# Kernel optimization log

Measured on AMD Instinct MI355X. Metric: run time of the kernel, lower is better.

Reference implementation:

```python
import jax, jax.numpy as jnp
import numpy as np

DIM = 768
HEADS = 12
HD = DIM // HEADS
SCALE = float(np.sqrt(HD))  # sqrt(dim // num_heads)


def layernorm(x, g, b, eps=1e-5):
    m = jnp.mean(x, axis=-1, keepdims=True)
    v = jnp.var(x, axis=-1, keepdims=True)
    return (x - m) * jax.lax.rsqrt(v + eps) * g + b


def dwconv(x, w, b, pad):
    # x: [B,C,H,W], w: [C,1,kh,kw] depthwise
    y = jax.lax.conv_general_dilated(
        x, w, window_strides=(1, 1), padding=[(pad, pad), (pad, pad)],
        feature_group_count=x.shape[1], dimension_numbers=('NCHW', 'OIHW', 'NCHW'))
    return y + b[None, :, None, None]


def mha(xq, xkv, wq, bq, wk, bk, wv, bv, wo, bo):
    # per-head Linears batched over heads; wq/wk/wv: [H, C, hd], biases [H, hd]
    B, N, C = xq.shape
    q = jnp.einsum('bnc,hcd->bhnd', xq, wq) + bq[None, :, None, :]
    k = jnp.einsum('bnc,hcd->bhnd', xkv, wk) + bk[None, :, None, :]
    v = jnp.einsum('bnc,hcd->bhnd', xkv, wv) + bv[None, :, None, :]
    z = jax.nn.sigmoid(jnp.einsum('bhnd,bhmd->bhnm', q, k) / SCALE)  # sigmoid, not softmax
    o = jnp.einsum('bhnm,bhmd->bhnd', z, v)
    o = o.transpose(0, 2, 1, 3).reshape(B, N, C)  # concat heads along feature dim
    return o @ wo + bo


def reference(decoder, wq1, bq1, wk1, bk1, wv1, bv1, wo1, bo1,
              wq2, bq2, wk2, bk2, wv2, bv2, wo2, bo2,
              alphas1, alphas2, peg_w, peg_b,
              ln1_g, ln1_b, ln2_g, ln2_b,
              cn_dw_w, cn_dw_b, cn_ln_g, cn_ln_b,
              cn_w1, cn_b1, cn_w2, cn_b2, cn_scale, cn_alphas):
    B, C, H, W = decoder.shape
    x = decoder.transpose(0, 2, 3, 1).reshape(B, H * W, C)  # [B,N,C]
    # block 1: alpha * x + MHA(x,x,x)
    x = alphas1 * x + mha(x, x, wq1, bq1, wk1, bk1, wv1, bv1, wo1, bo1)
    # PEG: depthwise 3x3 conv (replaces x, no residual in source)
    x4 = x.reshape(B, H, W, C).transpose(0, 3, 1, 2)
    x4 = dwconv(x4, peg_w, peg_b, pad=1)
    x = x4.transpose(0, 2, 3, 1).reshape(B, H * W, C)
    x = layernorm(x, ln1_g, ln1_b)
    # block 2 (encoder is None -> self-attention)
    x = alphas2 * x + mha(x, x, wq2, bq2, wk2, bk2, wv2, bv2, wo2, bo2)
    x = layernorm(x, ln2_g, ln2_b)
    x4 = x.reshape(B, H, W, C).transpose(0, 3, 1, 2)  # [B,C,H,W]
    # CNBlock head: dwconv7x7 -> LN -> Linear(4d) -> GELU -> Linear(d), layer_scale + alpha residual
    y = dwconv(x4, cn_dw_w, cn_dw_b, pad=3)
    y = y.transpose(0, 2, 3, 1)  # [B,H,W,C]
    y = layernorm(y, cn_ln_g, cn_ln_b)
    y = jax.nn.gelu(y @ cn_w1 + cn_b1, approximate=False)
    y = y @ cn_w2 + cn_b2
    y = y.transpose(0, 3, 1, 2)  # [B,C,H,W]
    out = cn_scale[None, :, None, None] * y + x4 * cn_alphas[None, :, None, None]
    return out


def setup_inputs() -> dict:
    key = jax.random.key(0)
    ks = iter(jax.random.split(key, 40))
    def n(shape, s=0.02):
        return jax.random.normal(next(ks), shape, dtype=jnp.float32) * s
    d = {}
    d['decoder'] = jax.random.normal(next(ks), (8, DIM, 32, 32), dtype=jnp.float32)
    for i in (1, 2):
        d[f'wq{i}'] = n((HEADS, DIM, HD)); d[f'bq{i}'] = n((HEADS, HD), 1e-6)
        d[f'wk{i}'] = n((HEADS, DIM, HD)); d[f'bk{i}'] = n((HEADS, HD), 1e-6)
        d[f'wv{i}'] = n((HEADS, DIM, HD)); d[f'bv{i}'] = n((HEADS, HD), 1e-6)
        d[f'wo{i}'] = n((DIM, DIM)); d[f'bo{i}'] = n((DIM,), 1e-6)
    d['alphas1'] = jnp.ones((DIM,), jnp.float32)
    d['alphas2'] = jnp.ones((DIM,), jnp.float32)
    d['peg_w'] = n((DIM, 1, 3, 3), 0.1); d['peg_b'] = n((DIM,), 1e-6)
    d['ln1_g'] = jnp.ones((DIM,), jnp.float32); d['ln1_b'] = jnp.zeros((DIM,), jnp.float32)
    d['ln2_g'] = jnp.ones((DIM,), jnp.float32); d['ln2_b'] = jnp.zeros((DIM,), jnp.float32)
    d['cn_dw_w'] = n((DIM, 1, 7, 7), 0.1); d['cn_dw_b'] = n((DIM,), 0.02)
    d['cn_ln_g'] = jnp.ones((DIM,), jnp.float32); d['cn_ln_b'] = jnp.zeros((DIM,), jnp.float32)
    d['cn_w1'] = n((DIM, 4 * DIM)); d['cn_b1'] = n((4 * DIM,), 0.02)
    d['cn_w2'] = n((4 * DIM, DIM)); d['cn_b2'] = n((DIM,), 0.02)
    d['cn_scale'] = jnp.full((DIM,), 1e-6, jnp.float32)
    d['cn_alphas'] = jnp.ones((DIM,), jnp.float32)
    return d
```

## Files before the change

kernel.cpp:

```cpp
#include <hip/hip_runtime.h>
#include <math.h>

#define BATCH 8
#define CDIM 768
#define NTOK 1024
#define NH 12
#define HDIM 64
#define QKVN 2304

typedef __attribute__((ext_vector_type(8))) short bf16x8;
typedef __attribute__((ext_vector_type(4))) float f32x4;

__device__ inline short f2bf(float f) {
    union { float f; unsigned u; } v; v.f = f;
    unsigned r = (v.u + 0x7FFF + ((v.u >> 16) & 1)) >> 16;
    return (short)r;
}

__device__ inline unsigned pack2bf(float lo, float hi) {
    return (unsigned)(unsigned short)f2bf(lo) | ((unsigned)(unsigned short)f2bf(hi) << 16);
}

__device__ inline void async_copy16(const short* g, short* l) {
    __builtin_amdgcn_global_load_lds(
        (const __attribute__((address_space(1))) void*)g,
        (__attribute__((address_space(3))) void*)l, 16, 0, 0);
}

__global__ __launch_bounds__(256) void k_prep(
    const float* __restrict__ wq1, const float* __restrict__ wk1, const float* __restrict__ wv1,
    const float* __restrict__ wq2, const float* __restrict__ wk2, const float* __restrict__ wv2,
    const float* __restrict__ wo1, const float* __restrict__ wo2,
    const float* __restrict__ cnw1, const float* __restrict__ cnw2,
    const float* __restrict__ bq1, const float* __restrict__ bk1, const float* __restrict__ bv1,
    const float* __restrict__ bq2, const float* __restrict__ bk2, const float* __restrict__ bv2,
    const float* __restrict__ dec,
    short* __restrict__ Wqkv1, short* __restrict__ Wqkv2,
    short* __restrict__ WoT1, short* __restrict__ WoT2,
    short* __restrict__ W1T, short* __restrict__ W2T,
    float* __restrict__ bqkv1, float* __restrict__ bqkv2,
    float* __restrict__ A0, short* __restrict__ Xb) {
    __shared__ float sh[64 * 65];
    int bid = blockIdx.x;
    int t = threadIdx.x;
    if (bid < 864) {
        int bx = bid % 12, z = bid / 12;
        int set = z / 36, rem = z % 36, sect = rem / 12, hh = rem % 12;
        const float* srcs[6] = {wq1, wk1, wv1, wq2, wk2, wv2};
        const float* src = srcs[set * 3 + sect] + (size_t)hh * 768 * 64;
        short* dst = (set ? Wqkv2 : Wqkv1) + ((size_t)sect * 768 + hh * 64) * 768;
        int k0 = bx * 64;
#pragma unroll
        for (int p = 0; p < 16; ++p) {
            int gid = t + p * 256;
            int r = gid >> 6, c = gid & 63;
            sh[r * 65 + c] = src[(size_t)(k0 + r) * 64 + c];
        }
        __syncthreads();
#pragma unroll
        for (int p = 0; p < 16; ++p) {
            int gid = t + p * 256;
            int d = gid >> 6, kk = gid & 63;
            dst[(size_t)d * 768 + k0 + kk] = f2bf(sh[kk * 65 + d]);
        }
    } else if (bid < 6624) {
        int r = bid - 864;
        const float* src; short* dst; int R, C, bx, by;
        if (r < 576)       { src = wo1;  dst = WoT1; R = 768;  C = 768;  bx = r % 24; by = r / 24; }
        else if (r < 1152) { int s = r - 576;  src = wo2;  dst = WoT2; R = 768;  C = 768;  bx = s % 24; by = s / 24; }
        else if (r < 3456) { int s = r - 1152; src = cnw1; dst = W1T;  R = 768;  C = 3072; bx = s % 96; by = s / 96; }
        else               { int s = r - 3456; src = cnw2; dst = W2T;  R = 3072; C = 768;  bx = s % 24; by = s / 24; }
        int c0 = bx * 32, r0 = by * 32, tx = t & 31, ty = t >> 5;
#pragma unroll
        for (int p = 0; p < 4; ++p)
            sh[(ty + p * 8) * 33 + tx] = src[(size_t)(r0 + ty + p * 8) * C + c0 + tx];
        __syncthreads();
#pragma unroll
        for (int p = 0; p < 4; ++p)
            dst[(size_t)(c0 + ty + p * 8) * R + r0 + tx] = f2bf(sh[tx * 33 + ty + p * 8]);
    } else if (bid < 6642) {
        int tid = (bid - 6624) * 256 + t;
        if (tid < 4608) {
            int set = tid / 2304, n = tid % 2304;
            int sect = n / 768, rem = n % 768;
            const float* srcs[6] = {bq1, bk1, bv1, bq2, bk2, bv2};
            float v = srcs[set * 3 + sect][rem];
            (set ? bqkv2 : bqkv1)[n] = v;
        }
    } else {
        int r = bid - 6642;
        int bx = r % 32, by = (r / 32) % 24, bz = r / 768;
        int n0 = bx * 32, c0 = by * 32, tx = t & 31, ty = t >> 5;
#pragma unroll
        for (int p = 0; p < 4; ++p) {
            int c = c0 + ty + p * 8;
            sh[(ty + p * 8) * 33 + tx] = dec[((size_t)bz * CDIM + c) * NTOK + n0 + tx];
        }
        __syncthreads();
#pragma unroll
        for (int p = 0; p < 4; ++p) {
            int n = n0 + ty + p * 8;
            float val = sh[tx * 33 + ty + p * 8];
            size_t idx = ((size_t)bz * NTOK + n) * CDIM + c0 + tx;
            A0[idx] = val;
            Xb[idx] = f2bf(val);
        }
    }
}

#define GM_FINAL 0
#define GM_PROJ  1
#define GM_GELU  2
#define GM_BF16  3

template<int MODE, int BN>
__global__ __launch_bounds__(256) void k_gemm_mfma(
    const short* __restrict__ A, const short* __restrict__ Bt,
    const float* __restrict__ bias, const float* __restrict__ resid,
    const float* __restrict__ rscale, const float* __restrict__ alph,
    float* __restrict__ outF, short* __restrict__ outB, int M, int N, int K) {
    constexpr int NT = BN / 32;
    constexpr int BP = BN / 64;
    constexpr int STAGE = 2 * 128 * 32 + 2 * BN * 32;
    constexpr int FINALS = (MODE == GM_FINAL) ? 64 * 132 * 2 : 0;
    constexpr int SMEM = STAGE > FINALS ? STAGE : FINALS;
    __shared__ short smem[SMEM];
    short* As = smem;
    short* Bs = smem + 2 * 128 * 32;
    int t = threadIdx.x;
    int w = t >> 6, lane = t & 63, l15 = lane & 15, quad = lane >> 4;
    int r0 = blockIdx.x * 128, n0 = blockIdx.y * BN;
    int wr = (w >> 1) * 64, wc = (w & 1) * (BN / 2);
    f32x4 acc[4][NT];
#pragma unroll
    for (int i = 0; i < 4; ++i)
#pragma unroll
        for (int j = 0; j < NT; ++j) acc[i][j] = (f32x4){0.f, 0.f, 0.f, 0.f};
    int sr = t >> 2, sc = ((t & 3) ^ ((sr >> 1) & 3)) * 8;
    const short* Ag = A + (size_t)(r0 + sr) * K + sc;
    const short* Bg = Bt + (size_t)(n0 + sr) * K + sc;
    short* AsW = As + w * 512;
    short* BsW = Bs + w * 512;
    int rsw = ((quad ^ ((l15 >> 1) & 3)) << 3);
#pragma unroll
    for (int p = 0; p < 2; ++p)
        async_copy16(Ag + (size_t)p * 64 * K, AsW + p * 2048);
#pragma unroll
    for (int p = 0; p < BP; ++p)
        async_copy16(Bg + (size_t)p * 64 * K, BsW + p * 2048);
    int st = 0;
    for (int k0 = 0; k0 < K; k0 += 32, st ^= 1) {
        __syncthreads();
        if (k0 + 32 < K) {
            int nst = st ^ 1;
#pragma unroll
            for (int p = 0; p < 2; ++p)
                async_copy16(Ag + k0 + 32 + (size_t)p * 64 * K,
                             AsW + nst * 4096 + p * 2048);
#pragma unroll
            for (int p = 0; p < BP; ++p)
                async_copy16(Bg + k0 + 32 + (size_t)p * 64 * K,
                             BsW + nst * (BN * 32) + p * 2048);
        }
        bf16x8 af[4], bf[NT];
#pragma unroll
        for (int i = 0; i < 4; ++i)
            af[i] = *(const bf16x8*)&As[st * 4096 + (wr + i * 16 + l15) * 32 + rsw];
#pragma unroll
        for (int j = 0; j < NT; ++j)
            bf[j] = *(const bf16x8*)&Bs[st * (BN * 32) + (wc + j * 16 + l15) * 32 + rsw];
#pragma unroll
        for (int i = 0; i < 4; ++i)
#pragma unroll
            for (int j = 0; j < NT; ++j)
                acc[i][j] = __builtin_amdgcn_mfma_f32_16x16x32_bf16(af[i], bf[j], acc[i][j], 0, 0, 0);
    }
    if (MODE == GM_FINAL) {
        __syncthreads();
        float* T = (float*)smem;
#pragma unroll
        for (int i = 0; i < 4; ++i)
#pragma unroll
            for (int j = 0; j < NT; ++j)
#pragma unroll
                for (int rr = 0; rr < 4; ++rr) {
                    int rl = wr + i * 16 + quad * 4 + rr;
                    int cl = wc + j * 16 + l15;
                    int row = r0 + rl, col = n0 + cl;
                    float val = acc[i][j][rr] + bias[col];
                    val = rscale[col] * val + alph[col] * resid[(size_t)row * N + col];
                    T[cl * 132 + rl] = val;
                }
        __syncthreads();
        int c = t >> 2, qo = (t & 3) * 32;
        int b = r0 >> 10, tokbase = r0 & 1023;
        float* obase = outF + ((size_t)(b * 768 + n0 + c)) * 1024 + tokbase + qo;
#pragma unroll
        for (int ii = 0; ii < 8; ++ii)
            *(float4*)&obase[ii * 4] = *(float4*)&T[c * 132 + qo + ii * 4];
        return;
    }
#pragma unroll
    for (int i = 0; i < 4; ++i)
#pragma unroll
        for (int j = 0; j < NT; ++j)
#pragma unroll
            for (int rr = 0; rr < 4; ++rr) {
                int row = r0 + wr + i * 16 + quad * 4 + rr;
                int col = n0 + wc + j * 16 + l15;
                float val = acc[i][j][rr] + bias[col];
                if (MODE == GM_PROJ) {
                    val += rscale[col] * resid[(size_t)row * N + col];
                    outF[(size_t)row * N + col] = val;
                } else if (MODE == GM_GELU) {
                    float u = val * (1.0f + 0.044715f * val * val);
                    float zz = __builtin_amdgcn_rcpf(
                        1.0f + __builtin_amdgcn_exp2f(-2.3022082f * u));
                    outB[(size_t)row * N + col] = f2bf(val * zz);
                } else {
                    outB[(size_t)row * N + col] = f2bf(val);
                }
            }
}

__global__ __launch_bounds__(256, 3) void k_attn_mfma(
    const short* __restrict__ q, const short* __restrict__ k,
    const short* __restrict__ v, short* __restrict__ o) {
    __shared__ short Ks[2][64 * 64];
    __shared__ short Vt[2][64][72];
    __shared__ short Ps[128][72];
    int t = threadIdx.x;
    int w = t >> 6, lane = t & 63, l15 = lane & 15, quad = lane >> 4;
    int flat = blockIdx.x + (blockIdx.y << 3) + blockIdx.z * 96;
    int xcd = flat & 7, slot = flat >> 3;
    int qb = slot & 7, grp = xcd * 12 + (slot >> 3);
    int h = grp % 12, b = grp / 12;
    int q0 = qb * 128;
    size_t base = ((size_t)b * NTOK) * QKVN + h * 64;
    const short* qp = q + base;
    const short* kp = k + base;
    const short* vp = v + base;

    bf16x8 qf[2][2];
#pragma unroll
    for (int nq = 0; nq < 2; ++nq)
#pragma unroll
        for (int kc = 0; kc < 2; ++kc)
            qf[nq][kc] = *(const bf16x8*)&qp[(size_t)(q0 + w * 32 + nq * 16 + l15) * QKVN + kc * 32 + quad * 8];

    int r8 = lane >> 3;
    const short* kg = kp + (size_t)r8 * QKVN + (((lane & 7) ^ r8) << 3);
    int vtok = t & 63, vd0 = (t >> 6) * 8;

    f32x4 oacc[4][2];
#pragma unroll
    for (int dt = 0; dt < 4; ++dt)
#pragma unroll
        for (int nq = 0; nq < 2; ++nq) oacc[dt][nq] = (f32x4){0.f, 0.f, 0.f, 0.f};

#pragma unroll
    for (int p = 0; p < 2; ++p)
        async_copy16(kg + (size_t)(p * 32 + w * 8) * QKVN, &Ks[0][(p * 32 + w * 8) * 64]);
    {
        bf16x8 v0 = *(const bf16x8*)&vp[(size_t)vtok * QKVN + vd0];
        bf16x8 v1 = *(const bf16x8*)&vp[(size_t)vtok * QKVN + vd0 + 32];
#pragma unroll
        for (int j = 0; j < 8; ++j) {
            Vt[0][vd0 + j][vtok] = v0[j];
            Vt[0][vd0 + 32 + j][vtok] = v1[j];
        }
    }

    short* prow0 = &Ps[w * 32 + l15][0];
    short* prow1 = &Ps[w * 32 + 16 + l15][0];

    for (int kt = 0; kt < 16; ++kt) {
        int cur = kt & 1, nxt = cur ^ 1;
        __syncthreads();
        bf16x8 vv0, vv1;
        if (kt < 15) {
            const short* kgn = kg + (size_t)((kt + 1) * 64) * QKVN;
#pragma unroll
            for (int p = 0; p < 2; ++p)
                async_copy16(kgn + (size_t)(p * 32 + w * 8) * QKVN, &Ks[nxt][(p * 32 + w * 8) * 64]);
            vv0 = *(const bf16x8*)&vp[((size_t)((kt + 1) * 64 + vtok)) * QKVN + vd0];
            vv1 = *(const bf16x8*)&vp[((size_t)((kt + 1) * 64 + vtok)) * QKVN + vd0 + 32];
        }
        f32x4 sacc[4][2];
#pragma unroll
        for (int mk = 0; mk < 4; ++mk)
#pragma unroll
            for (int nq = 0; nq < 2; ++nq) sacc[mk][nq] = (f32x4){0.f, 0.f, 0.f, 0.f};
        __builtin_amdgcn_s_setprio(1);
#pragma unroll
        for (int mk = 0; mk < 4; ++mk)
#pragma unroll
            for (int kc = 0; kc < 2; ++kc) {
                bf16x8 kf = *(const bf16x8*)&Ks[cur][(mk * 16 + l15) * 64 + (((kc * 4 + quad) ^ (l15 & 7)) << 3)];
#pragma unroll
                for (int nq = 0; nq < 2; ++nq)
                    sacc[mk][nq] = __builtin_amdgcn_mfma_f32_16x16x32_bf16(kf, qf[nq][kc], sacc[mk][nq], 0, 0, 0);
            }
        __builtin_amdgcn_s_setprio(0);
#pragma unroll
        for (int mk = 0; mk < 4; ++mk)
#pragma unroll
            for (int nq = 0; nq < 2; ++nq) {
                float z[4];
#pragma unroll
                for (int rr = 0; rr < 4; ++rr)
                    z[rr] = __builtin_amdgcn_rcpf(
                        1.0f + __builtin_amdgcn_exp2f(sacc[mk][nq][rr] * -0.18033688011112042f));
                unsigned* pw = (unsigned*)((nq ? prow1 : prow0) + mk * 16 + quad * 4);
                pw[0] = pack2bf(z[0], z[1]);
                pw[1] = pack2bf(z[2], z[3]);
            }
        if (kt < 15) {
#pragma unroll
            for (int j = 0; j < 8; ++j) {
                Vt[nxt][vd0 + j][vtok] = vv0[j];
                Vt[nxt][vd0 + 32 + j][vtok] = vv1[j];
            }
        }
        asm volatile("s_waitcnt lgkmcnt(0)" ::: "memory");
        __builtin_amdgcn_sched_barrier(0);
        bf16x8 pf[2][2];
#pragma unroll
        for (int kc = 0; kc < 2; ++kc)
#pragma unroll
            for (int nq = 0; nq < 2; ++nq)
                pf[kc][nq] = *(const bf16x8*)((nq ? prow1 : prow0) + kc * 32 + quad * 8);
        __builtin_amdgcn_s_setprio(1);
#pragma unroll
        for (int dt = 0; dt < 4; ++dt)
#pragma unroll
            for (int kc = 0; kc < 2; ++kc) {
                bf16x8 vf = *(const bf16x8*)&Vt[cur][dt * 16 + l15][kc * 32 + quad * 8];
#pragma unroll
                for (int nq = 0; nq < 2; ++nq)
                    oacc[dt][nq] = __builtin_amdgcn_mfma_f32_16x16x32_bf16(vf, pf[kc][nq], oacc[dt][nq], 0, 0, 0);
            }
        __builtin_amdgcn_s_setprio(0);
    }
#pragma unroll
    for (int dt = 0; dt < 4; ++dt)
#pragma unroll
        for (int nq = 0; nq < 2; ++nq) {
            int tok = q0 + w * 32 + nq * 16 + l15;
            int c = h * 64 + dt * 16 + quad * 4;
            unsigned* op = (unsigned*)&o[((size_t)b * NTOK + tok) * CDIM + c];
            op[0] = pack2bf(oacc[dt][nq][0], oacc[dt][nq][1]);
            op[1] = pack2bf(oacc[dt][nq][2], oacc[dt][nq][3]);
        }
}

template<int K>
__global__ __launch_bounds__(256) void k_dwconv_t(
    const float* __restrict__ in, const float* __restrict__ w,
    const float* __restrict__ bias, float* __restrict__ out) {
    constexpr int PAD = K / 2;
    constexpr int KK = K * K;
    int t = threadIdx.x;
    int c = blockIdx.y * 64 + (t & 63);
    int j = blockIdx.x * 4 + (t >> 6);
    int b = blockIdx.z;
    float wr[KK];
#pragma unroll
    for (int qq = 0; qq < KK; ++qq) wr[qq] = w[(size_t)c * KK + qq];
    float bsv = bias[c];
    const float* base = in + (size_t)b * NTOK * CDIM + c;
    float win[K][K];
#pragma unroll
    for (int s = 1; s < K; ++s) {
        int ii = s - 1 - PAD;
#pragma unroll
        for (int qq = 0; qq < K; ++qq) {
            int jj = j - PAD + qq;
            win[s][qq] = (ii >= 0 && jj >= 0 && jj < 32)
                         ? base[(size_t)(ii * 32 + jj) * CDIM] : 0.0f;
        }
    }
#pragma unroll
    for (int i = 0; i < 32; ++i) {
#pragma unroll
        for (int r = 0; r < K - 1; ++r)
#pragma unroll
            for (int qq = 0; qq < K; ++qq) win[r][qq] = win[r + 1][qq];
        int ii = i + PAD;
#pragma unroll
        for (int qq = 0; qq < K; ++qq) {
            int jj = j - PAD + qq;
            win[K - 1][qq] = (ii < 32 && jj >= 0 && jj < 32)
                             ? base[(size_t)(ii * 32 + jj) * CDIM] : 0.0f;
        }
        float acc = bsv;
#pragma unroll
        for (int r = 0; r < K; ++r)
#pragma unroll
            for (int qq = 0; qq < K; ++qq)
                acc = fmaf(win[r][qq], wr[r * K + qq], acc);
        out[((size_t)b * NTOK + i * 32 + j) * CDIM + c] = acc;
    }
}

__global__ __launch_bounds__(256) void k_ln(
    const float* __restrict__ in, const float* __restrict__ g,
    const float* __restrict__ b, float* __restrict__ outF, short* __restrict__ outB) {
    int row = blockIdx.x;
    const float* xr = in + (size_t)row * CDIM;
    int t = threadIdx.x;
    float x0 = xr[t], x1 = xr[t + 256], x2 = xr[t + 512];
    float s = x0 + x1 + x2;
    float sq = x0 * x0 + x1 * x1 + x2 * x2;
#pragma unroll
    for (int off = 32; off > 0; off >>= 1) {
        s += __shfl_down(s, off);
        sq += __shfl_down(sq, off);
    }
    __shared__ float ws[4], wq2[4];
    int wid = t >> 6, lane = t & 63;
    if (lane == 0) { ws[wid] = s; wq2[wid] = sq; }
    __syncthreads();
    if (t == 0) {
        float S = ws[0] + ws[1] + ws[2] + ws[3];
        float Q = wq2[0] + wq2[1] + wq2[2] + wq2[3];
        float m = S * (1.0f / CDIM);
        float var = Q * (1.0f / CDIM) - m * m;
        ws[0] = m;
        wq2[0] = rsqrtf(var + 1e-5f);
    }
    __syncthreads();
    float m = ws[0], inv = wq2[0];
    float y0 = (x0 - m) * inv * g[t] + b[t];
    float y1 = (x1 - m) * inv * g[t + 256] + b[t + 256];
    float y2 = (x2 - m) * inv * g[t + 512] + b[t + 512];
    if (outF) {
        float* orow = outF + (size_t)row * CDIM;
        orow[t] = y0; orow[t + 256] = y1; orow[t + 512] = y2;
    }
    if (outB) {
        short* orow = outB + (size_t)row * CDIM;
        orow[t] = f2bf(y0); orow[t + 256] = f2bf(y1); orow[t + 512] = f2bf(y2);
    }
}

extern "C" void kernel_launch(void* const* d_in, const int* in_sizes, int n_in,
                              void* d_out, int out_size, void* d_ws, size_t ws_size,
                              hipStream_t stream) {
    const float* dec = (const float*)d_in[0];
    const float* wq1 = (const float*)d_in[1]; const float* bq1 = (const float*)d_in[2];
    const float* wk1 = (const float*)d_in[3]; const float* bk1 = (const float*)d_in[4];
    const float* wv1 = (const float*)d_in[5]; const float* bv1 = (const float*)d_in[6];
    const float* wo1 = (const float*)d_in[7]; const float* bo1 = (const float*)d_in[8];
    const float* wq2 = (const float*)d_in[9]; const float* bq2 = (const float*)d_in[10];
    const float* wk2 = (const float*)d_in[11]; const float* bk2 = (const float*)d_in[12];
    const float* wv2 = (const float*)d_in[13]; const float* bv2 = (const float*)d_in[14];
    const float* wo2 = (const float*)d_in[15]; const float* bo2 = (const float*)d_in[16];
    const float* alphas1 = (const float*)d_in[17];
    const float* alphas2 = (const float*)d_in[18];
    const float* peg_w = (const float*)d_in[19]; const float* peg_b = (const float*)d_in[20];
    const float* ln1_g = (const float*)d_in[21]; const float* ln1_b = (const float*)d_in[22];
    const float* ln2_g = (const float*)d_in[23]; const float* ln2_b = (const float*)d_in[24];
    const float* cn_dw_w = (const float*)d_in[25]; const float* cn_dw_b = (const float*)d_in[26];
    const float* cn_ln_g = (const float*)d_in[27]; const float* cn_ln_b = (const float*)d_in[28];
    const float* cn_w1 = (const float*)d_in[29]; const float* cn_b1 = (const float*)d_in[30];
    const float* cn_w2 = (const float*)d_in[31]; const float* cn_b2 = (const float*)d_in[32];
    const float* cn_scale = (const float*)d_in[33]; const float* cn_alphas = (const float*)d_in[34];
    float* out = (float*)d_out;

    const size_t S = (size_t)BATCH * NTOK * CDIM;
    float* A0 = (float*)d_ws;
    float* A1 = A0 + S;
    short* Xb  = (short*)(A1 + S);
    short* QKV = Xb + S;
    short* Ob  = QKV + 3 * S;
    short* Hb  = Ob + S;
    short* Wqkv1 = Hb + 2 * S;
    short* Wqkv2 = Wqkv1 + 2304 * 768;
    short* WoT1  = Wqkv2 + 2304 * 768;
    short* WoT2  = WoT1 + 768 * 768;
    short* W1T   = WoT2 + 768 * 768;
    short* W2T   = W1T + (size_t)3072 * 768;
    float* bqkv1 = (float*)(W2T + (size_t)768 * 3072);
    float* bqkv2 = bqkv1 + 2304;
    short* Hfull = QKV + 2 * S;

    dim3 dwgrid(8, 12, 8);

    k_prep<<<dim3(12786), 256, 0, stream>>>(
        wq1, wk1, wv1, wq2, wk2, wv2, wo1, wo2, cn_w1, cn_w2,
        bq1, bk1, bv1, bq2, bk2, bv2, dec,
        Wqkv1, Wqkv2, WoT1, WoT2, W1T, W2T, bqkv1, bqkv2, A0, Xb);

    k_gemm_mfma<GM_BF16, 128><<<dim3(64, 18), 256, 0, stream>>>(
        Xb, Wqkv1, bqkv1, nullptr, nullptr, nullptr, nullptr, QKV, 8192, 2304, 768);
    k_attn_mfma<<<dim3(8, 12, 8), 256, 0, stream>>>(QKV, QKV + 768, QKV + 1536, Ob);
    k_gemm_mfma<GM_PROJ, 64><<<dim3(64, 12), 256, 0, stream>>>(
        Ob, WoT1, bo1, A0, alphas1, nullptr, A1, nullptr, 8192, 768, 768);
    k_dwconv_t<3><<<dwgrid, 256, 0, stream>>>(A1, peg_w, peg_b, A0);
    k_ln<<<8192, 256, 0, stream>>>(A0, ln1_g, ln1_b, A1, Xb);

    k_gemm_mfma<GM_BF16, 128><<<dim3(64, 18), 256, 0, stream>>>(
        Xb, Wqkv2, bqkv2, nullptr, nullptr, nullptr, nullptr, QKV, 8192, 2304, 768);
    k_attn_mfma<<<dim3(8, 12, 8), 256, 0, stream>>>(QKV, QKV + 768, QKV + 1536, Ob);
    k_gemm_mfma<GM_PROJ, 64><<<dim3(64, 12), 256, 0, stream>>>(
        Ob, WoT2, bo2, A1, alphas2, nullptr, A0, nullptr, 8192, 768, 768);
    k_ln<<<8192, 256, 0, stream>>>(A0, ln2_g, ln2_b, A1, nullptr);

    k_dwconv_t<7><<<dwgrid, 256, 0, stream>>>(A1, cn_dw_w, cn_dw_b, A0);
    k_ln<<<8192, 256, 0, stream>>>(A0, cn_ln_g, cn_ln_b, nullptr, Xb);
    k_gemm_mfma<GM_GELU, 128><<<dim3(64, 24), 256, 0, stream>>>(
        Xb, W1T, cn_b1, nullptr, nullptr, nullptr, nullptr, Hfull, 8192, 3072, 768);
    k_gemm_mfma<GM_FINAL, 64><<<dim3(64, 12), 256, 0, stream>>>(
        Hfull, W2T, cn_b2, A1, cn_scale, cn_alphas, out, nullptr, 8192, 768, 3072);
}
```

Baseline: 565.9 us.

## Add 128x256-tile triple-buffered GEMM kernel for QKV, projection and GELU GEMMs

Introduces a new 512-thread GEMM kernel with 128x256 output tiles, a K step of 64 and a three-stage asynchronous LDS pipeline using explicit vmcnt waits. It replaces the old 256-thread 128x128/128x64 GEMM for the QKV, output-projection and first MLP GEMMs. The old kernel is cut down to the final transposed-output mode only. Larger tiles raise data reuse and deeper prefetch hides latency, but the projection GEMM now launches only 192 blocks, which may leave compute units underused. LDS per block is about 144 KB, which limits occupancy.

```diff
diff --git a/kernel.cpp b/kernel.cpp
--- a/kernel.cpp
+++ b/kernel.cpp
@@ -108,10 +108,98 @@
     }
 }
 
+#define G3_BF16 0
+#define G3_GELU 1
+#define G3_PROJ 2
+
+template<int MODE>
+__global__ __launch_bounds__(512) void k_gemm3s(
+    const short* __restrict__ A, const short* __restrict__ Bt,
+    const float* __restrict__ bias, const float* __restrict__ resid,
+    const float* __restrict__ rscale,
+    float* __restrict__ outF, short* __restrict__ outB, int M, int N, int K) {
+    __shared__ short As[3][2][128 * 32];
+    __shared__ short Bs[3][2][256 * 32];
+    int t = threadIdx.x;
+    int w = t >> 6, lane = t & 63, l15 = lane & 15, quad = lane >> 4;
+    int r0 = blockIdx.x * 128, n0 = blockIdx.y * 256;
+    int wrow = (w >> 2) * 64, wcol = (w & 3) * 64;
+    f32x4 acc[4][4];
+#pragma unroll
+    for (int i = 0; i < 4; ++i)
+#pragma unroll
+        for (int j = 0; j < 4; ++j) acc[i][j] = (f32x4){0.f, 0.f, 0.f, 0.f};
+    int sr = t >> 2, sc = ((t & 3) ^ ((sr >> 1) & 3)) * 8;
+    const short* Ag = A + (size_t)(r0 + sr) * K + sc;
+    const short* Bg = Bt + (size_t)(n0 + sr) * K + sc;
+    int rsw = ((quad ^ ((l15 >> 1) & 3)) << 3);
+    int NT = K >> 6;
+
+    auto ISSUE = [&](int buf, int k0) {
+#pragma unroll
+        for (int ks = 0; ks < 2; ++ks) {
+            async_copy16(Ag + k0 + ks * 32, &As[buf][ks][w * 512]);
+#pragma unroll
+            for (int p = 0; p < 2; ++p)
+                async_copy16(Bg + (size_t)p * 128 * K + k0 + ks * 32,
+                             &Bs[buf][ks][p * 4096 + w * 512]);
+        }
+    };
+    ISSUE(0, 0);
+    ISSUE(1, 64);
+    for (int tt = 0; tt < NT; ++tt) {
+        int buf = tt % 3;
+        if (tt + 1 < NT) {
+            asm volatile("s_waitcnt vmcnt(6)" ::: "memory");
+        } else {
+            asm volatile("s_waitcnt vmcnt(0)" ::: "memory");
+        }
+        __builtin_amdgcn_s_barrier();
+        __builtin_amdgcn_sched_barrier(0);
+        if (tt + 2 < NT) ISSUE((tt + 2) % 3, (tt + 2) * 64);
+        bf16x8 af[4][2], bf[4][2];
+#pragma unroll
+        for (int i = 0; i < 4; ++i)
+#pragma unroll
+            for (int ks = 0; ks < 2; ++ks)
+                af[i][ks] = *(const bf16x8*)&As[buf][ks][(wrow + i * 16 + l15) * 32 + rsw];
+#pragma unroll
+        for (int j = 0; j < 4; ++j)
+#pragma unroll
+            for (int ks = 0; ks < 2; ++ks)
+                bf[j][ks] = *(const bf16x8*)&Bs[buf][ks][(wcol + j * 16 + l15) * 32 + rsw];
+#pragma unroll
+        for (int ks = 0; ks < 2; ++ks)
+#pragma unroll
+            for (int i = 0; i < 4; ++i)
+#pragma unroll
+                for (int j = 0; j < 4; ++j)
+                    acc[i][j] = __builtin_amdgcn_mfma_f32_16x16x32_bf16(af[i][ks], bf[j][ks], acc[i][j], 0, 0, 0);
+    }
+#pragma unroll
+    for (int i = 0; i < 4; ++i)
+#pragma unroll
+        for (int j = 0; j < 4; ++j)
+#pragma unroll
+            for (int rr = 0; rr < 4; ++rr) {
+                int row = r0 + wrow + i * 16 + quad * 4 + rr;
+                int col = n0 + wcol + j * 16 + l15;
+                float val = acc[i][j][rr] + bias[col];
+                if (MODE == G3_PROJ) {
+                    val += rscale[col] * resid[(size_t)row * N + col];
+                    outF[(size_t)row * N + col] = val;
+                } else if (MODE == G3_GELU) {
+                    float u = val * (1.0f + 0.044715f * val * val);
+                    float zz = __builtin_amdgcn_rcpf(
+                        1.0f + __builtin_amdgcn_exp2f(-2.3022082f * u));
+                    outB[(size_t)row * N + col] = f2bf(val * zz);
+                } else {
+                    outB[(size_t)row * N + col] = f2bf(val);
+                }
+            }
+}
+
 #define GM_FINAL 0
-#define GM_PROJ  1
-#define GM_GELU  2
-#define GM_BF16  3
 
 template<int MODE, int BN>
 __global__ __launch_bounds__(256) void k_gemm_mfma(
@@ -175,52 +263,28 @@
             for (int j = 0; j < NT; ++j)
                 acc[i][j] = __builtin_amdgcn_mfma_f32_16x16x32_bf16(af[i], bf[j], acc[i][j], 0, 0, 0);
     }
-    if (MODE == GM_FINAL) {
-        __syncthreads();
-        float* T = (float*)smem;
-#pragma unroll
-        for (int i = 0; i < 4; ++i)
-#pragma unroll
-            for (int j = 0; j < NT; ++j)
-#pragma unroll
-                for (int rr = 0; rr < 4; ++rr) {
-                    int rl = wr + i * 16 + quad * 4 + rr;
-                    int cl = wc + j * 16 + l15;
-                    int row = r0 + rl, col = n0 + cl;
-                    float val = acc[i][j][rr] + bias[col];
-                    val = rscale[col] * val + alph[col] * resid[(size_t)row * N + col];
-                    T[cl * 132 + rl] = val;
-                }
-        __syncthreads();
-        int c = t >> 2, qo = (t & 3) * 32;
-        int b = r0 >> 10, tokbase = r0 & 1023;
-        float* obase = outF + ((size_t)(b * 768 + n0 + c)) * 1024 + tokbase + qo;
-#pragma unroll
-        for (int ii = 0; ii < 8; ++ii)
-            *(float4*)&obase[ii * 4] = *(float4*)&T[c * 132 + qo + ii * 4];
-        return;
-    }
+    __syncthreads();
+    float* T = (float*)smem;
 #pragma unroll
     for (int i = 0; i < 4; ++i)
 #pragma unroll
         for (int j = 0; j < NT; ++j)
 #pragma unroll
             for (int rr = 0; rr < 4; ++rr) {
-                int row = r0 + wr + i * 16 + quad * 4 + rr;
-                int col = n0 + wc + j * 16 + l15;
+                int rl = wr + i * 16 + quad * 4 + rr;
+                int cl = wc + j * 16 + l15;
+                int row = r0 + rl, col = n0 + cl;
                 float val = acc[i][j][rr] + bias[col];
-                if (MODE == GM_PROJ) {
-                    val += rscale[col] * resid[(size_t)row * N + col];
-                    outF[(size_t)row * N + col] = val;
-                } else if (MODE == GM_GELU) {
-                    float u = val * (1.0f + 0.044715f * val * val);
-                    float zz = __builtin_amdgcn_rcpf(
-                        1.0f + __builtin_amdgcn_exp2f(-2.3022082f * u));
-                    outB[(size_t)row * N + col] = f2bf(val * zz);
-                } else {
-                    outB[(size_t)row * N + col] = f2bf(val);
-                }
+                val = rscale[col] * val + alph[col] * resid[(size_t)row * N + col];
+                T[cl * 132 + rl] = val;
             }
+    __syncthreads();
+    int c = t >> 2, qo = (t & 3) * 32;
+    int b = r0 >> 10, tokbase = r0 & 1023;
+    float* obase = outF + ((size_t)(b * 768 + n0 + c)) * 1024 + tokbase + qo;
+#pragma unroll
+    for (int ii = 0; ii < 8; ++ii)
+        *(float4*)&obase[ii * 4] = *(float4*)&T[c * 132 + qo + ii * 4];
 }
 
 __global__ __launch_bounds__(256, 3) void k_attn_mfma(
@@ -492,25 +556,25 @@
         bq1, bk1, bv1, bq2, bk2, bv2, dec,
         Wqkv1, Wqkv2, WoT1, WoT2, W1T, W2T, bqkv1, bqkv2, A0, Xb);
 
-    k_gemm_mfma<GM_BF16, 128><<<dim3(64, 18), 256, 0, stream>>>(
-        Xb, Wqkv1, bqkv1, nullptr, nullptr, nullptr, nullptr, QKV, 8192, 2304, 768);
+    k_gemm3s<G3_BF16><<<dim3(64, 9), 512, 0, stream>>>(
+        Xb, Wqkv1, bqkv1, nullptr, nullptr, nullptr, QKV, 8192, 2304, 768);
     k_attn_mfma<<<dim3(8, 12, 8), 256, 0, stream>>>(QKV, QKV + 768, QKV + 1536, Ob);
-    k_gemm_mfma<GM_PROJ, 64><<<dim3(64, 12), 256, 0, stream>>>(
-        Ob, WoT1, bo1, A0, alphas1, nullptr, A1, nullptr, 8192, 768, 768);
+    k_gemm3s<G3_PROJ><<<dim3(64, 3), 512, 0, stream>>>(
+        Ob, WoT1, bo1, A0, alphas1, A1, nullptr, 8192, 768, 768);
     k_dwconv_t<3><<<dwgrid, 256, 0, stream>>>(A1, peg_w, peg_b, A0);
     k_ln<<<8192, 256, 0, stream>>>(A0, ln1_g, ln1_b, A1, Xb);
 
-    k_gemm_mfma<GM_BF16, 128><<<dim3(64, 18), 256, 0, stream>>>(
-        Xb, Wqkv2, bqkv2, nullptr, nullptr, nullptr, nullptr, QKV, 8192, 2304, 768);
+    k_gemm3s<G3_BF16><<<dim3(64, 9), 512, 0, stream>>>(
+        Xb, Wqkv2, bqkv2, nullptr, nullptr, nullptr, QKV, 8192, 2304, 768);
     k_attn_mfma<<<dim3(8, 12, 8), 256, 0, stream>>>(QKV, QKV + 768, QKV + 1536, Ob);
-    k_gemm_mfma<GM_PROJ, 64><<<dim3(64, 12), 256, 0, stream>>>(
-        Ob, WoT2, bo2, A1, alphas2, nullptr, A0, nullptr, 8192, 768, 768);
+    k_gemm3s<G3_PROJ><<<dim3(64, 3), 512, 0, stream>>>(
+        Ob, WoT2, bo2, A1, alphas2, A0, nullptr, 8192, 768, 768);
     k_ln<<<8192, 256, 0, stream>>>(A0, ln2_g, ln2_b, A1, nullptr);
 
     k_dwconv_t<7><<<dwgrid, 256, 0, stream>>>(A1, cn_dw_w, cn_dw_b, A0);
     k_ln<<<8192, 256, 0, stream>>>(A0, cn_ln_g, cn_ln_b, nullptr, Xb);
-    k_gemm_mfma<GM_GELU, 128><<<dim3(64, 24), 256, 0, stream>>>(
-        Xb, W1T, cn_b1, nullptr, nullptr, nullptr, nullptr, Hfull, 8192, 3072, 768);
+    k_gemm3s<G3_GELU><<<dim3(64, 12), 512, 0, stream>>>(
+        Xb, W1T, cn_b1, nullptr, nullptr, nullptr, Hfull, 8192, 3072, 768);
     k_gemm_mfma<GM_FINAL, 64><<<dim3(64, 12), 256, 0, stream>>>(
         Hfull, W2T, cn_b2, A1, cn_scale, cn_alphas, out, nullptr, 8192, 768, 3072);
 }
```

Result: slower. 636.8 us (+12.5%).

## Use three-stage LDS pipeline with partial vmcnt waits in MFMA GEMM

Applied to the files above, without the earlier changes.

Replaces the double-buffered global-to-LDS async copy loop with a triple-buffered ring, issuing loads two K-steps ahead. Explicit s_waitcnt vmcnt with a partial count lets the current stage be consumed while the next stage's loads are still in flight, and a raw s_barrier replaces __syncthreads. This is meant to hide global load latency better, at the cost of more LDS per block, which may reduce occupancy. It also relies on a hand-counted number of outstanding loads per thread.

```diff
diff --git a/kernel.cpp b/kernel.cpp
--- a/kernel.cpp
+++ b/kernel.cpp
@@ -121,12 +121,13 @@
     float* __restrict__ outF, short* __restrict__ outB, int M, int N, int K) {
     constexpr int NT = BN / 32;
     constexpr int BP = BN / 64;
-    constexpr int STAGE = 2 * 128 * 32 + 2 * BN * 32;
+    constexpr int ASTG = 128 * 32;
+    constexpr int BSTG = BN * 32;
+    constexpr int SSTG = ASTG + BSTG;
+    constexpr int STAGE = 3 * SSTG;
     constexpr int FINALS = (MODE == GM_FINAL) ? 64 * 132 * 2 : 0;
     constexpr int SMEM = STAGE > FINALS ? STAGE : FINALS;
     __shared__ short smem[SMEM];
-    short* As = smem;
-    short* Bs = smem + 2 * 128 * 32;
     int t = threadIdx.x;
     int w = t >> 6, lane = t & 63, l15 = lane & 15, quad = lane >> 4;
     int r0 = blockIdx.x * 128, n0 = blockIdx.y * BN;
@@ -139,41 +140,49 @@
     int sr = t >> 2, sc = ((t & 3) ^ ((sr >> 1) & 3)) * 8;
     const short* Ag = A + (size_t)(r0 + sr) * K + sc;
     const short* Bg = Bt + (size_t)(n0 + sr) * K + sc;
-    short* AsW = As + w * 512;
-    short* BsW = Bs + w * 512;
     int rsw = ((quad ^ ((l15 >> 1) & 3)) << 3);
-#pragma unroll
-    for (int p = 0; p < 2; ++p)
-        async_copy16(Ag + (size_t)p * 64 * K, AsW + p * 2048);
-#pragma unroll
-    for (int p = 0; p < BP; ++p)
-        async_copy16(Bg + (size_t)p * 64 * K, BsW + p * 2048);
-    int st = 0;
-    for (int k0 = 0; k0 < K; k0 += 32, st ^= 1) {
-        __syncthreads();
-        if (k0 + 32 < K) {
-            int nst = st ^ 1;
-#pragma unroll
-            for (int p = 0; p < 2; ++p)
-                async_copy16(Ag + k0 + 32 + (size_t)p * 64 * K,
-                             AsW + nst * 4096 + p * 2048);
-#pragma unroll
-            for (int p = 0; p < BP; ++p)
-                async_copy16(Bg + k0 + 32 + (size_t)p * 64 * K,
-                             BsW + nst * (BN * 32) + p * 2048);
-        }
+    int wo = w * 512;
+
+    auto ISSUE = [&](int s, int k0) {
+        short* base = smem + s * SSTG;
+#pragma unroll
+        for (int p = 0; p < 2; ++p)
+            async_copy16(Ag + k0 + (size_t)p * 64 * K, base + p * 2048 + wo);
+#pragma unroll
+        for (int p = 0; p < BP; ++p)
+            async_copy16(Bg + k0 + (size_t)p * 64 * K, base + ASTG + p * 2048 + wo);
+    };
+    int NI = K >> 5;
+    ISSUE(0, 0);
+    ISSUE(1, 32);
+    int cur = 0;
+    for (int it = 0; it < NI; ++it) {
+        if (it + 1 < NI) {
+            if constexpr (BP == 2) asm volatile("s_waitcnt vmcnt(4)" ::: "memory");
+            else                   asm volatile("s_waitcnt vmcnt(3)" ::: "memory");
+        } else {
+            asm volatile("s_waitcnt vmcnt(0)" ::: "memory");
+        }
+        __builtin_amdgcn_s_barrier();
+        __builtin_amdgcn_sched_barrier(0);
+        if (it + 2 < NI) {
+            int nxt = cur + 2; if (nxt >= 3) nxt -= 3;
+            ISSUE(nxt, (it + 2) * 32);
+        }
+        short* base = smem + cur * SSTG;
         bf16x8 af[4], bf[NT];
 #pragma unroll
         for (int i = 0; i < 4; ++i)
-            af[i] = *(const bf16x8*)&As[st * 4096 + (wr + i * 16 + l15) * 32 + rsw];
+            af[i] = *(const bf16x8*)&base[(wr + i * 16 + l15) * 32 + rsw];
 #pragma unroll
         for (int j = 0; j < NT; ++j)
-            bf[j] = *(const bf16x8*)&Bs[st * (BN * 32) + (wc + j * 16 + l15) * 32 + rsw];
+            bf[j] = *(const bf16x8*)&base[ASTG + (wc + j * 16 + l15) * 32 + rsw];
 #pragma unroll
         for (int i = 0; i < 4; ++i)
 #pragma unroll
             for (int j = 0; j < NT; ++j)
                 acc[i][j] = __builtin_amdgcn_mfma_f32_16x16x32_bf16(af[i], bf[j], acc[i][j], 0, 0, 0);
+        if (++cur == 3) cur = 0;
     }
     if (MODE == GM_FINAL) {
         __syncthreads();
```

After: 585.0 us. +3.4%, slower.
